# Kernel optimization log

Measured on AMD Instinct MI355X. Metric: run time of the kernel, lower is better.

## Reference

```python
import jax, jax.numpy as jnp
import numpy as np
from jax.scipy.special import xlogy

B, N, F_IN, D, L = 32, 512, 20, 128, 5
NEG = -1e7


def setup_inputs() -> dict:
    key = jax.random.key(0)
    ks = jax.random.split(key, 24)
    s = lambda n: 1.0 / np.sqrt(n)
    inp = {}
    inp["fatoms"] = jax.random.normal(ks[0], (B, N, F_IN), jnp.float32)
    # normalized dense multi-relation adjacency (row sums ~1 for stability)
    inp["adj"] = jax.random.uniform(ks[1], (B, N, N, 3), jnp.float32) * (2.0 / N)
    inp["all_mask"] = jnp.ones((B, N, 1), jnp.float32)
    inp["current_mask"] = jnp.ones((B, N, 1), jnp.float32)
    inp["prob_mask"] = jnp.ones((B, N, 1), jnp.float32)
    inp["focus"] = jax.random.randint(ks[2], (B, 1), 0, N)
    inp["action_batch"] = jax.random.randint(ks[3], (B, 3), 0, 2)
    # embeddings (bias-free Linear(20, D))
    inp["W_emb"] = jax.random.normal(ks[4], (F_IN, D)) * s(F_IN)
    inp["W_cemb"] = jax.random.normal(ks[5], (F_IN, D)) * s(F_IN)
    # per-iteration, per-relation GCN weights [L,3,D,D] and biases [L,3,D]
    inp["actor_W"] = jax.random.normal(ks[6], (L, 3, D, D)) * s(D)
    inp["actor_b"] = jnp.zeros((L, 3, D), jnp.float32)
    inp["critic_W"] = jax.random.normal(ks[7], (L, 3, D, D)) * s(D)
    inp["critic_b"] = jnp.zeros((L, 3, D), jnp.float32)
    # end_selection_layer: Linear(2D,D)+ReLU+Linear(D,1,no bias)
    inp["We1"] = jax.random.normal(ks[8], (2 * D, D)) * s(2 * D)
    inp["be1"] = jnp.zeros((D,), jnp.float32)
    inp["We2"] = jax.random.normal(ks[9], (D, 1)) * s(D)
    # bond_selection_layer: Linear(2D,D)+ReLU+Linear(D,3,no bias)+Softmax
    inp["Wb1"] = jax.random.normal(ks[10], (2 * D, D)) * s(2 * D)
    inp["bb1"] = jnp.zeros((D,), jnp.float32)
    inp["Wb2"] = jax.random.normal(ks[11], (D, 3)) * s(D)
    # stop_selection_layer: Linear(D,D)+ReLU+Linear(D,2,no bias)+Softmax
    inp["Ws1"] = jax.random.normal(ks[12], (D, D)) * s(D)
    inp["bs1"] = jnp.zeros((D,), jnp.float32)
    inp["Ws2"] = jax.random.normal(ks[13], (D, 2)) * s(D)
    # qlayer: Linear(2D,D)+ReLU+Linear(D,1)
    inp["Wq1"] = jax.random.normal(ks[14], (2 * D, D)) * s(2 * D)
    inp["bq1"] = jnp.zeros((D,), jnp.float32)
    inp["Wq2"] = jax.random.normal(ks[15], (D, 1)) * s(D)
    inp["bq2"] = jnp.zeros((1,), jnp.float32)
    return inp


def _entropy(p):
    return -jnp.sum(xlogy(p, p), axis=-1)


def reference(fatoms, adj, all_mask, current_mask, prob_mask, focus, action_batch,
              W_emb, W_cemb, actor_W, actor_b, critic_W, critic_b,
              We1, be1, We2, Wb1, bb1, Wb2, Ws1, bs1, Ws2, Wq1, bq1, Wq2, bq2):
    def gcn_stack(x, Ws_all, bs_all):
        def step(h, wb):
            W, b = wb  # [3,D,D], [3,D]
            hw = jnp.einsum('bmd,rde->rbme', h, W) + b[:, None, None, :]
            msg = jax.nn.relu(jnp.einsum('bnmr,rbme->rbne', adj, hw))
            return jnp.sum(msg, axis=0) * all_mask, None
        h, _ = jax.lax.scan(step, x, (Ws_all, bs_all))
        return h

    # actor and critic feature updates
    x_a = gcn_stack(jax.nn.relu(fatoms @ W_emb), actor_W, actor_b)   # [B,N,D]
    x_c = gcn_stack(jax.nn.relu(fatoms @ W_cemb), critic_W, critic_b)

    # maxpool_sumpool + qlayer
    max_mask = jnp.where(current_mask == 1.0, 0.0, NEG)
    sum_pool = jnp.sum(x_c * current_mask, axis=1)                   # [B,D]
    max_pool = jnp.max(x_c + max_mask, axis=1)                       # [B,D]
    q_in = jnp.concatenate([sum_pool, max_pool], axis=-1)            # [B,2D]
    qvalue = jax.nn.relu(q_in @ Wq1 + bq1) @ Wq2 + bq2               # [B,1]

    pm = jnp.where(prob_mask == 1.0, 0.0, NEG)                       # [B,N,1]
    b, n, d = x_a.shape
    start = jnp.take_along_axis(x_a, jnp.broadcast_to(focus[:, :, None], (b, 1, d)), axis=1)  # [B,1,D]

    end_input = jnp.concatenate([jnp.broadcast_to(start, (b, n, d)), x_a], axis=-1)           # [B,N,2D]
    logits = jax.nn.relu(end_input @ We1 + be1) @ We2 + pm           # [B,N,1]
    end_probs = jax.nn.softmax(logits, axis=1)[..., 0]               # [B,N]

    end_idx = action_batch[:, 0:1]
    end_atom = jnp.take_along_axis(x_a, jnp.broadcast_to(end_idx[:, :, None], (b, 1, d)), axis=1)
    end_prob_new = jnp.take_along_axis(end_probs, end_idx, axis=1)   # [B,1]

    bond_in = jnp.concatenate([start, end_atom], axis=-1)[:, 0, :]   # [B,2D]
    bond_probs = jax.nn.softmax(jax.nn.relu(bond_in @ Wb1 + bb1) @ Wb2, axis=-1)  # [B,3]
    bond_prob_new = jnp.take_along_axis(bond_probs, action_batch[:, 1:2], axis=1)

    stop_probs = jax.nn.softmax(jax.nn.relu(start[:, 0, :] @ Ws1 + bs1) @ Ws2, axis=-1)  # [B,2]
    stop_prob_new = jnp.take_along_axis(stop_probs, action_batch[:, 2:3], axis=1)

    prob_batch_new = jnp.concatenate([end_prob_new, bond_prob_new, stop_prob_new], axis=-1)  # [B,3]
    entropy = _entropy(end_probs) + _entropy(bond_probs) + _entropy(stop_probs)             # [B]
    return prob_batch_new, entropy, qvalue
```

## Files before the change

kernel.cpp:

```cpp
#include <hip/hip_runtime.h>
#include <cstdint>
#include <cstddef>

typedef unsigned short u16;
typedef __bf16 bfx8 __attribute__((ext_vector_type(8)));
typedef float f32x4 __attribute__((ext_vector_type(4)));

#define NEGV -10000000.0f
constexpr int cB = 32, cN = 512, cD = 128, cF = 20, cL = 5;

__device__ __forceinline__ float bf2f(u16 h){ unsigned u = ((unsigned)h)<<16; return __builtin_bit_cast(float,u); }
__device__ __forceinline__ u16 f2bf(float f){ unsigned u = __builtin_bit_cast(unsigned,f); return (u16)((u + 0x7fffu + ((u>>16)&1u))>>16); }

constexpr int WOF_EMB  = 0;
constexpr int WOF_CEMB = 2560;
constexpr int WOF_AW   = 5120;
constexpr int WOF_CW   = 250880;
constexpr int WOF_WE1  = 496640;
constexpr int WOF_WE2  = 529408;
constexpr int WOF_WB1  = 529536;
constexpr int WOF_WB2  = 562304;
constexpr int WOF_WS1  = 562688;
constexpr int WOF_WS2  = 579072;
constexpr int WOF_WQ1  = 579328;
constexpr int WOF_WQ2  = 612096;
constexpr int WTOTAL   = 612224;

struct WPtrs { const void* p[12]; };

__global__ __launch_bounds__(256) void canon_w(WPtrs wp, u16* __restrict__ Wc){
  __shared__ int s_flag;
  int t = threadIdx.x;
  if (t == 0) s_flag = 0;
  __syncthreads();
  const u16* probe = (const u16*)wp.p[2];
  int big = 0;
  #pragma unroll
  for (int i=0;i<2;++i){
    float a = fabsf(bf2f(probe[i*256 + t]));
    if (!(a < 1e10f)) big = 1;
  }
  if (__any(big)) s_flag = 1;
  __syncthreads();
  int flag = s_flag;
  int i = blockIdx.x*256 + t;
  if (i >= WTOTAL) return;
  constexpr int offs[13] = {WOF_EMB, WOF_CEMB, WOF_AW, WOF_CW, WOF_WE1, WOF_WE2,
                            WOF_WB1, WOF_WB2, WOF_WS1, WOF_WS2, WOF_WQ1, WOF_WQ2, WTOTAL};
  int a = 0;
  #pragma unroll
  for (int k = 1; k < 12; ++k) if (i >= offs[k]) a = k;
  int off = i - offs[a];
  const void* p = wp.p[a];
  Wc[i] = flag ? f2bf(((const float*)p)[off]) : ((const u16*)p)[off];
}

__global__ __launch_bounds__(256) void prep_adj(const float* __restrict__ adj, u16* __restrict__ adjT){
  int idx = blockIdx.x*256 + threadIdx.x;
  int m8 = idx & 63; int bn = idx >> 6;
  const float* src = adj + ((size_t)bn*512 + (size_t)m8*8)*3;
  float v[24];
  #pragma unroll
  for (int q=0;q<6;++q) ((float4*)v)[q] = ((const float4*)src)[q];
  __align__(16) u16 o[3][8];
  #pragma unroll
  for (int j=0;j<24;++j) o[j%3][j/3] = f2bf(v[j]);
  #pragma unroll
  for (int r=0;r<3;++r){
    size_t off = ((size_t)r*16384 + (size_t)bn)*512 + (size_t)m8*8;
    *reinterpret_cast<int4*>(adjT + off) = *reinterpret_cast<const int4*>(&o[r][0]);
  }
}

__global__ __launch_bounds__(256) void prep_w(const u16* __restrict__ Wc, u16* __restrict__ WT){
  __shared__ u16 sh[128*129];
  int blk = blockIdx.x;
  const u16* in;
  if (blk < 30){
    int s = blk/15; int lr = blk%15;
    in = Wc + (s ? WOF_CW : WOF_AW) + (size_t)lr*16384;
  } else {
    in = Wc + WOF_WE1 + 128*cD;
  }
  u16* out = WT + (size_t)blk*16384;
  int t = threadIdx.x;
  #pragma unroll 4
  for (int i=0;i<64;++i){ int idx=i*256+t; int d=idx>>7, e=idx&127; sh[e*129+d]=in[idx]; }
  __syncthreads();
  #pragma unroll 4
  for (int i=0;i<64;++i){ int idx=i*256+t; int e=idx>>7, d=idx&127; out[idx]=sh[e*129+d]; }
}

__global__ __launch_bounds__(128) void emb(const float* __restrict__ fatoms, const u16* __restrict__ Wc, u16* __restrict__ h0){
  int row = blockIdx.x;
  int s = row >> 14; int bn = row & 16383;
  __shared__ float fa[cF];
  int t = threadIdx.x;
  if (t < cF) fa[t] = fatoms[(size_t)bn*cF + t];
  __syncthreads();
  const u16* W = Wc + (s ? WOF_CEMB : WOF_EMB);
  float acc = 0.f;
  #pragma unroll
  for (int f=0; f<cF; ++f) acc += fa[f]*bf2f(W[f*cD + t]);
  h0[((size_t)s*cB*cN + bn)*cD + t] = f2bf(fmaxf(acc,0.f));
}

__device__ __forceinline__ void stage16k(const u16* gbase, int ldaB, int ktB, char* sm, int w, int l){
  #pragma unroll
  for (int i=0;i<4;++i){
    int c = (w<<2) + i;
    int row = (c<<3) + (l>>3);
    const char* src = (const char*)gbase + (size_t)row*ldaB + ktB + (((l&7)^(row&7))<<4);
    __builtin_amdgcn_global_load_lds((const __attribute__((address_space(1))) void*)src,
                                     (__attribute__((address_space(3))) void*)(sm + (c<<10)), 16, 0, 0);
  }
}
__device__ __forceinline__ void stage8k(const u16* gbase, int ldaB, int ktB, char* sm, int w, int l){
  #pragma unroll
  for (int i=0;i<2;++i){
    int c = (w<<1) + i;
    int row = (c<<3) + (l>>3);
    const char* src = (const char*)gbase + (size_t)row*ldaB + ktB + (((l&7)^(row&7))<<4);
    __builtin_amdgcn_global_load_lds((const __attribute__((address_space(1))) void*)src,
                                     (__attribute__((address_space(3))) void*)(sm + (c<<10)), 16, 0, 0);
  }
}
__device__ __forceinline__ bfx8 readfrag(const char* sm, int row, int kk, int l){
  int col = ((kk<<6) + ((l>>4)<<4)) ^ ((row&7)<<4);
  return *(const bfx8*)(sm + row*128 + col);
}
template<int MF,int NF>
__device__ __forceinline__ void mfma_tile(const char* A, const char* Bm, int ra, int rb, int l, f32x4 (&acc)[MF][NF]){
  #pragma unroll
  for (int kk=0; kk<2; ++kk){
    bfx8 af[MF], bv[NF];
    #pragma unroll
    for (int f=0; f<MF; ++f) af[f] = readfrag(A,  ra+(f<<4)+(l&15), kk, l);
    #pragma unroll
    for (int f=0; f<NF; ++f) bv[f] = readfrag(Bm, rb+(f<<4)+(l&15), kk, l);
    #pragma unroll
    for (int mf=0; mf<MF; ++mf)
      #pragma unroll
      for (int nf=0; nf<NF; ++nf)
        acc[mf][nf] = __builtin_amdgcn_mfma_f32_16x16x32_bf16(af[mf], bv[nf], acc[mf][nf], 0,0,0);
  }
}

__global__ __launch_bounds__(256,2) void k1_hw(const u16* __restrict__ WT, const u16* __restrict__ h,
                                               const float* __restrict__ actor_b, const float* __restrict__ critic_b,
                                               u16* __restrict__ hwT, int layer){
  __shared__ __align__(16) char smA[16384];
  __shared__ __align__(16) char smB[16384];
  int blk = blockIdx.x;
  int nt = blk & 3; int srb = blk >> 2;
  int s = srb/96; int rb = srb%96; int r = rb>>5; int b = rb&31;
  int t = threadIdx.x, w = t>>6, l = t&63, wr = w>>1, wc = w&1;
  const u16* Abase = WT + (size_t)(s*15 + layer*3 + r)*16384;
  const u16* Bbase = h + ((size_t)s*cB*cN + (size_t)b*cN + (size_t)nt*128)*cD;
  f32x4 acc[4][4];
  #pragma unroll
  for (int i=0;i<4;++i){ acc[i][0]=f32x4{0,0,0,0}; acc[i][1]=f32x4{0,0,0,0}; acc[i][2]=f32x4{0,0,0,0}; acc[i][3]=f32x4{0,0,0,0}; }
  for (int kt=0; kt<2; ++kt){
    __syncthreads();
    stage16k(Abase, 256, kt*128, smA, w, l);
    stage16k(Bbase, 256, kt*128, smB, w, l);
    __syncthreads();
    mfma_tile<4,4>(smA, smB, wr<<6, wc<<6, l, acc);
  }
  const float* bias = (s ? critic_b : actor_b) + (layer*3 + r)*cD;
  u16* outB = hwT + (size_t)((s*3+r)*cB + b)*cD*cN;
  #pragma unroll
  for (int mf=0; mf<4; ++mf)
    #pragma unroll
    for (int nf=0; nf<4; ++nf)
      #pragma unroll
      for (int j=0; j<4; ++j){
        int e = (wr<<6) + (mf<<4) + ((l>>4)<<2) + j;
        int m = nt*128 + (wc<<6) + (nf<<4) + (l&15);
        outB[(size_t)e*cN + m] = f2bf(acc[mf][nf][j] + bias[e]);
      }
}

__global__ __launch_bounds__(256,2) void k2f(const u16* __restrict__ adjT, const u16* __restrict__ hwT_in,
                                             u16* __restrict__ hwT_out, const float* __restrict__ all_mask,
                                             const u16* __restrict__ WT,
                                             const float* __restrict__ actor_b, const float* __restrict__ critic_b,
                                             u16* __restrict__ hfin, int layer){
  __shared__ __align__(16) char smA[8192];
  __shared__ __align__(16) char smB[16384];
  __shared__ __align__(16) char smW[16384];
  __shared__ __align__(16) char hT[2][8192];
  int blk = blockIdx.x;
  int xcd = blk & 7; int slot = blk >> 3;
  int b = (slot>>4)*8 + xcd;
  int rest = slot & 15; int s = rest>>3; int mt = rest&7;
  int t = threadIdx.x, w = t>>6, l = t&63, wr = w>>1, wc = w&1;
  f32x4 sum[2][4];
  #pragma unroll
  for (int i=0;i<2;++i)
    #pragma unroll
    for (int j=0;j<4;++j) sum[i][j]=f32x4{0,0,0,0};
  for (int r=0; r<3; ++r){
    f32x4 acc[2][4];
    #pragma unroll
    for (int i=0;i<2;++i)
      #pragma unroll
      for (int j=0;j<4;++j) acc[i][j]=f32x4{0,0,0,0};
    const u16* Abase = adjT + ((size_t)(r*cB + b)*cN + (size_t)mt*64)*cN;
    const u16* Bbase = hwT_in + (size_t)((s*3+r)*cB + b)*cD*cN;
    for (int kt=0; kt<8; ++kt){
      __syncthreads();
      stage8k (Abase, 1024, kt*128, smA, w, l);
      stage16k(Bbase, 1024, kt*128, smB, w, l);
      __syncthreads();
      mfma_tile<2,4>(smA, smB, wr<<5, wc<<6, l, acc);
    }
    #pragma unroll
    for (int mf=0; mf<2; ++mf)
      #pragma unroll
      for (int nf=0; nf<4; ++nf)
        #pragma unroll
        for (int j=0; j<4; ++j)
          sum[mf][nf][j] += fmaxf(acc[mf][nf][j], 0.f);
  }
  #pragma unroll
  for (int mf=0; mf<2; ++mf)
    #pragma unroll
    for (int nf=0; nf<4; ++nf)
      #pragma unroll
      for (int j=0; j<4; ++j){
        int nl = (wr<<5) + (mf<<4) + ((l>>4)<<2) + j;
        int e  = (wc<<6) + (nf<<4) + (l&15);
        int n  = mt*64 + nl;
        u16 hv = f2bf(sum[mf][nf][j] * all_mask[b*cN + n]);
        char* dst = hT[e>>6] + nl*128 + (((e&63)*2) ^ ((nl&7)<<4));
        *(u16*)dst = hv;
        if (layer == cL-1) hfin[((size_t)(s*cB + b)*cN + n)*cD + e] = hv;
      }
  if (layer < cL-1){
    for (int r=0; r<3; ++r){
      __syncthreads();
      const u16* Wbase = WT + (size_t)(s*15 + (layer+1)*3 + r)*16384;
      stage16k(Wbase, 256, 0,   smB, w, l);
      stage16k(Wbase, 256, 128, smW, w, l);
      __syncthreads();
      f32x4 acc2[4][2];
      #pragma unroll
      for (int i=0;i<4;++i){ acc2[i][0]=f32x4{0,0,0,0}; acc2[i][1]=f32x4{0,0,0,0}; }
      mfma_tile<4,2>(smB, hT[0], wr<<6, wc<<5, l, acc2);
      mfma_tile<4,2>(smW, hT[1], wr<<6, wc<<5, l, acc2);
      const float* bias = (s ? critic_b : actor_b) + ((layer+1)*3 + r)*cD;
      u16* outB = hwT_out + (size_t)((s*3+r)*cB + b)*cD*cN;
      #pragma unroll
      for (int mf=0; mf<4; ++mf)
        #pragma unroll
        for (int nf=0; nf<2; ++nf)
          #pragma unroll
          for (int j=0; j<4; ++j){
            int e = (wr<<6) + (mf<<4) + ((l>>4)<<2) + j;
            int m = mt*64 + (wc<<5) + (nf<<4) + (l&15);
            outB[(size_t)e*cN + m] = f2bf(acc2[mf][nf][j] + bias[e]);
          }
    }
  }
}

__global__ __launch_bounds__(256) void pool_part(const u16* __restrict__ xc, const float* __restrict__ cmask,
                                                 float* __restrict__ part){
  int blk = blockIdx.x;
  int b = blk >> 4, c = blk & 15;
  int t = threadIdx.x; int d = t & 127, nh = t >> 7;
  const u16* x = xc + ((size_t)b*cN + c*32 + nh*16)*cD;
  const float* cm = cmask + (size_t)b*cN + c*32 + nh*16;
  float sm = 0.f, mx = -3e38f;
  #pragma unroll
  for (int i=0;i<16;++i){
    float v = bf2f(x[(size_t)i*cD + d]);
    float m = cm[i];
    sm += v*m;
    mx = fmaxf(mx, v + (m==1.0f ? 0.f : NEGV));
  }
  __shared__ float s_sm[2][128], s_mx[2][128];
  s_sm[nh][d] = sm; s_mx[nh][d] = mx;
  __syncthreads();
  if (nh == 0){
    float* dst = part + ((size_t)b*16 + c)*256;
    dst[d]       = sm + s_sm[1][d];
    dst[128 + d] = fmaxf(mx, s_mx[1][d]);
  }
}

__global__ __launch_bounds__(128) void start_vec(const u16* __restrict__ xa, const int* __restrict__ focus,
                                                 const int* __restrict__ action, const u16* __restrict__ Wc,
                                                 const float* __restrict__ be1,
                                                 float* __restrict__ startv, float* __restrict__ endv, float* __restrict__ sc){
  int b = blockIdx.x, t = threadIdx.x;
  __shared__ float s_sh[128];
  const u16* We1 = Wc + WOF_WE1;
  int f = focus[b];
  int e0 = action[b*3 + 0];
  float sv = bf2f(xa[((size_t)b*cN + f)*cD + t]);
  startv[b*cD + t] = sv;
  endv[b*cD + t] = bf2f(xa[((size_t)b*cN + e0)*cD + t]);
  s_sh[t] = sv;
  __syncthreads();
  float acc = be1[t];
  #pragma unroll 4
  for (int k=0;k<128;++k) acc += s_sh[k]*bf2f(We1[k*cD + t]);
  sc[b*cD + t] = acc;
}

__global__ __launch_bounds__(256,2) void end_logits2(const u16* __restrict__ xa, const u16* __restrict__ WT,
                                                     const float* __restrict__ sc, const u16* __restrict__ Wc,
                                                     const float* __restrict__ prob_mask, float* __restrict__ logits){
  __shared__ __align__(16) char smA[16384];
  __shared__ __align__(16) char smB[16384];
  __shared__ float sh_sc[128], sh_w2[128], rowsum[2][128];
  int blk = blockIdx.x;
  int nt = blk & 3, b = blk >> 2;
  int t = threadIdx.x, w = t>>6, l = t&63, wr = w>>1, wc = w&1;
  if (t < 128){ sh_sc[t] = sc[b*cD + t]; sh_w2[t] = bf2f(Wc[WOF_WE2 + t]); }
  const u16* Abase = xa + ((size_t)b*cN + (size_t)nt*128)*cD;
  const u16* Bbase = WT + (size_t)30*16384;
  f32x4 acc[4][4];
  #pragma unroll
  for (int i=0;i<4;++i){ acc[i][0]=f32x4{0,0,0,0}; acc[i][1]=f32x4{0,0,0,0}; acc[i][2]=f32x4{0,0,0,0}; acc[i][3]=f32x4{0,0,0,0}; }
  for (int kt=0; kt<2; ++kt){
    __syncthreads();
    stage16k(Abase, 256, kt*128, smA, w, l);
    stage16k(Bbase, 256, kt*128, smB, w, l);
    __syncthreads();
    mfma_tile<4,4>(smA, smB, wr<<6, wc<<6, l, acc);
  }
  float p[4][4];
  #pragma unroll
  for (int mf=0;mf<4;++mf)
    #pragma unroll
    for (int j=0;j<4;++j) p[mf][j] = 0.f;
  #pragma unroll
  for (int mf=0; mf<4; ++mf)
    #pragma unroll
    for (int nf=0; nf<4; ++nf){
      int e = (wc<<6) + (nf<<4) + (l&15);
      float scv = sh_sc[e], w2 = sh_w2[e];
      #pragma unroll
      for (int j=0; j<4; ++j)
        p[mf][j] += fmaxf(acc[mf][nf][j] + scv, 0.f) * w2;
    }
  #pragma unroll
  for (int mf=0; mf<4; ++mf)
    #pragma unroll
    for (int j=0; j<4; ++j){
      float v = p[mf][j];
      #pragma unroll
      for (int o=1;o<16;o<<=1) v += __shfl_xor(v, o, 64);
      if ((l&15)==0) rowsum[wc][(wr<<6) + (mf<<4) + ((l>>4)<<2) + j] = v;
    }
  __syncthreads();
  if (t < 128){
    int n = nt*128 + t;
    float pm = (prob_mask[b*cN + n]==1.0f) ? 0.f : NEGV;
    logits[b*cN + n] = rowsum[0][t] + rowsum[1][t] + pm;
  }
}

__global__ __launch_bounds__(128) void heads_final(const float* __restrict__ part, const u16* __restrict__ Wc,
                                                   const float* __restrict__ bq1, const float* __restrict__ bq2,
                                                   const float* __restrict__ logits, const int* __restrict__ action,
                                                   const float* __restrict__ startv, const float* __restrict__ endv,
                                                   const float* __restrict__ bb1, const float* __restrict__ bs1,
                                                   float* __restrict__ out){
  int b = blockIdx.x, t = threadIdx.x;
  __shared__ float qin[256];
  __shared__ float sv[128], ev[128];
  __shared__ float redq[2], red5[5][2];
  __shared__ float HendSh;
  sv[t] = startv[b*cD + t];
  ev[t] = endv[b*cD + t];
  float sm = 0.f, mx = -3e38f;
  #pragma unroll
  for (int c=0;c<16;++c){
    const float* src = part + ((size_t)b*16 + c)*256;
    sm += src[t];
    mx = fmaxf(mx, src[128 + t]);
  }
  qin[t] = sm; qin[128+t] = mx;
  __syncthreads();
  float acc = bq1[t];
  #pragma unroll 4
  for (int k=0; k<256; ++k) acc += qin[k]*bf2f(Wc[WOF_WQ1 + k*cD + t]);
  float hc = fmaxf(acc,0.f)*bf2f(Wc[WOF_WQ2 + t]);
  #pragma unroll
  for (int o=32;o>0;o>>=1) hc += __shfl_down(hc, o, 64);
  if ((t&63)==0) redq[t>>6] = hc;
  if (t < 64){
    float v[8];
    #pragma unroll
    for (int i=0;i<8;++i) v[i] = logits[b*cN + i*64 + t];
    float m = v[0];
    #pragma unroll
    for (int i=1;i<8;++i) m = fmaxf(m, v[i]);
    #pragma unroll
    for (int o=32;o>0;o>>=1) m = fmaxf(m, __shfl_xor(m, o, 64));
    float e[8]; float s = 0.f;
    #pragma unroll
    for (int i=0;i<8;++i){ e[i] = expf(v[i]-m); s += e[i]; }
    #pragma unroll
    for (int o=32;o>0;o>>=1) s += __shfl_xor(s, o, 64);
    float lns = logf(s);
    float pl = 0.f;
    #pragma unroll
    for (int i=0;i<8;++i){ float p = e[i]/s; pl += p*((v[i]-m) - lns); }
    #pragma unroll
    for (int o=32;o>0;o>>=1) pl += __shfl_xor(pl, o, 64);
    int idx = action[b*3 + 0];
    if (t == (idx & 63)){
      float pe = 0.f;
      #pragma unroll
      for (int i=0;i<8;++i) if ((idx>>6)==i) pe = e[i];
      out[b*3 + 0] = pe / s;
    }
    if (t == 0) HendSh = -pl;
  }
  float ab = bb1[t], as_ = bs1[t];
  #pragma unroll 4
  for (int k=0;k<128;++k){ float svk = sv[k]; ab += svk*bf2f(Wc[WOF_WB1 + k*cD + t]); as_ += svk*bf2f(Wc[WOF_WS1 + k*cD + t]); }
  #pragma unroll 4
  for (int k=0;k<128;++k) ab += ev[k]*bf2f(Wc[WOF_WB1 + (128+k)*cD + t]);
  float hb = fmaxf(ab,0.f), hs = fmaxf(as_,0.f);
  float r0 = hb*bf2f(Wc[WOF_WB2 + t*3+0]);
  float r1 = hb*bf2f(Wc[WOF_WB2 + t*3+1]);
  float r2 = hb*bf2f(Wc[WOF_WB2 + t*3+2]);
  float r3 = hs*bf2f(Wc[WOF_WS2 + t*2+0]);
  float r4 = hs*bf2f(Wc[WOF_WS2 + t*2+1]);
  #pragma unroll
  for (int o=32;o>0;o>>=1){
    r0 += __shfl_xor(r0,o,64); r1 += __shfl_xor(r1,o,64); r2 += __shfl_xor(r2,o,64);
    r3 += __shfl_xor(r3,o,64); r4 += __shfl_xor(r4,o,64);
  }
  if ((t&63)==0){ int wid=t>>6; red5[0][wid]=r0; red5[1][wid]=r1; red5[2][wid]=r2; red5[3][wid]=r3; red5[4][wid]=r4; }
  __syncthreads();
  if (t==0){
    out[128 + b] = redq[0] + redq[1] + bq2[0];
    auto xlx = [](float p){ return p > 0.f ? p*logf(p) : 0.f; };
    float bl0=red5[0][0]+red5[0][1], bl1=red5[1][0]+red5[1][1], bl2=red5[2][0]+red5[2][1];
    float sl0=red5[3][0]+red5[3][1], sl1=red5[4][0]+red5[4][1];
    float m = fmaxf(fmaxf(bl0,bl1),bl2);
    float e0=expf(bl0-m), e1=expf(bl1-m), e2=expf(bl2-m); float S=e0+e1+e2;
    float p0=e0/S, p1=e1/S, p2=e2/S;
    float Hb = -(xlx(p0) + xlx(p1) + xlx(p2));
    int a1 = action[b*3+1];
    out[b*3+1] = (a1==0)?p0:((a1==1)?p1:p2);
    float ms = fmaxf(sl0,sl1);
    float f0=expf(sl0-ms), f1=expf(sl1-ms); float T=f0+f1;
    float q0=f0/T, q1=f1/T;
    float Hs = -(xlx(q0) + xlx(q1));
    int a2 = action[b*3+2];
    out[b*3+2] = (a2==0)?q0:q1;
    out[96+b] = HendSh + Hb + Hs;
  }
}

extern "C" void kernel_launch(void* const* d_in, const int* in_sizes, int n_in,
                              void* d_out, int out_size, void* d_ws, size_t ws_size,
                              hipStream_t stream){
  const float* fatoms      = (const float*)d_in[0];
  const float* adj         = (const float*)d_in[1];
  const float* all_mask    = (const float*)d_in[2];
  const float* current_mask= (const float*)d_in[3];
  const float* prob_mask   = (const float*)d_in[4];
  const int*   focus       = (const int*)d_in[5];
  const int*   action      = (const int*)d_in[6];
  const float* actor_b     = (const float*)d_in[10];
  const float* critic_b    = (const float*)d_in[12];
  const float* be1         = (const float*)d_in[14];
  const float* bb1         = (const float*)d_in[17];
  const float* bs1         = (const float*)d_in[20];
  const float* bq1         = (const float*)d_in[23];
  const float* bq2         = (const float*)d_in[25];

  char* ws = (char*)d_ws;
  size_t o = 0;
  u16* adjT = (u16*)(ws + o);  o += (size_t)3*cB*cN*cN*2;
  u16* WT   = (u16*)(ws + o);  o += (size_t)31*16384*2;
  u16* hbuf = (u16*)(ws + o);  o += (size_t)2*2*cB*cN*cD*2;
  u16* hwT0 = (u16*)(ws + o);  o += (size_t)2*3*cB*cD*cN*2;
  u16* hwT1 = (u16*)(ws + o);  o += (size_t)2*3*cB*cD*cN*2;
  u16* Wcan = (u16*)(ws + o);  o += (size_t)WTOTAL*2;
  float* part   = (float*)(ws + o); o += (size_t)cB*16*256*4;
  float* logits = (float*)(ws + o); o += (size_t)cB*cN*4;
  float* sc     = (float*)(ws + o); o += (size_t)cB*cD*4;
  float* startv = (float*)(ws + o); o += (size_t)cB*cD*4;
  float* endv   = (float*)(ws + o); o += (size_t)cB*cD*4;
  float* out = (float*)d_out;

  WPtrs wp;
  wp.p[0]=d_in[7];  wp.p[1]=d_in[8];  wp.p[2]=d_in[9];  wp.p[3]=d_in[11];
  wp.p[4]=d_in[13]; wp.p[5]=d_in[15]; wp.p[6]=d_in[16]; wp.p[7]=d_in[18];
  wp.p[8]=d_in[19]; wp.p[9]=d_in[21]; wp.p[10]=d_in[22]; wp.p[11]=d_in[24];

  canon_w<<<dim3((WTOTAL+255)/256), dim3(256), 0, stream>>>(wp, Wcan);
  prep_adj<<<dim3(4096), dim3(256), 0, stream>>>(adj, adjT);
  prep_w<<<dim3(31), dim3(256), 0, stream>>>(Wcan, WT);
  emb<<<dim3(2*cB*cN), dim3(128), 0, stream>>>(fatoms, Wcan, hbuf);

  const size_t hstride = (size_t)2*cB*cN*cD;
  u16* hfin = hbuf + hstride;
  k1_hw<<<dim3(768), dim3(256), 0, stream>>>(WT, hbuf, actor_b, critic_b, hwT0, 0);
  for (int l=0; l<cL; ++l){
    u16* win  = (l&1) ? hwT1 : hwT0;
    u16* wout = (l&1) ? hwT0 : hwT1;
    k2f<<<dim3(512), dim3(256), 0, stream>>>(adjT, win, wout, all_mask, WT, actor_b, critic_b, hfin, l);
  }
  const u16* xa = hfin;
  const u16* xc = hfin + (size_t)cB*cN*cD;

  start_vec<<<dim3(cB), dim3(128), 0, stream>>>(xa, focus, action, Wcan, be1, startv, endv, sc);
  end_logits2<<<dim3(cB*4), dim3(256), 0, stream>>>(xa, WT, sc, Wcan, prob_mask, logits);
  pool_part<<<dim3(cB*16), dim3(256), 0, stream>>>(xc, current_mask, part);
  heads_final<<<dim3(cB), dim3(128), 0, stream>>>(part, Wcan, bq1, bq2, logits, action, startv, endv, bb1, bs1, out);
}
```

Before: 260.0 us.

## Double-buffer adjacency and hw tiles in k2f with async staged loads

Flattens the three relation loops and eight k-tiles in k2f into one 24-step loop. The shared tiles become two buffers, so global loads for the next tile are issued before the MFMA work on the current one, using explicit vmcnt waits and raw barriers in place of __syncthreads. The weight-staging phase reuses the now double-sized smB buffer instead of a separate smW, which keeps LDS usage roughly the same. This relies on stage8k/stage16k issuing exactly the expected number of vector memory ops for vmcnt(6) to be correct, so a mismatch would cause data races.

```diff
diff --git a/kernel.cpp b/kernel.cpp
--- a/kernel.cpp
+++ b/kernel.cpp
@@ -186,42 +186,52 @@
                                              const u16* __restrict__ WT,
                                              const float* __restrict__ actor_b, const float* __restrict__ critic_b,
                                              u16* __restrict__ hfin, int layer){
-  __shared__ __align__(16) char smA[8192];
-  __shared__ __align__(16) char smB[16384];
-  __shared__ __align__(16) char smW[16384];
+  __shared__ __align__(16) char smA[2][8192];
+  __shared__ __align__(16) char smB[2][16384];
   __shared__ __align__(16) char hT[2][8192];
   int blk = blockIdx.x;
   int xcd = blk & 7; int slot = blk >> 3;
   int b = (slot>>4)*8 + xcd;
   int rest = slot & 15; int s = rest>>3; int mt = rest&7;
   int t = threadIdx.x, w = t>>6, l = t&63, wr = w>>1, wc = w&1;
-  f32x4 sum[2][4];
+  const u16* adjB = adjT + ((size_t)b*cN + (size_t)mt*64)*cN;
+  const u16* hwB  = hwT_in + (size_t)(s*3*cB + b)*cD*cN;
+  const size_t adjRs = (size_t)cB*cN*cN;
+  const size_t hwRs  = (size_t)cB*cD*cN;
+  f32x4 sum[2][4], acc[2][4];
   #pragma unroll
   for (int i=0;i<2;++i)
     #pragma unroll
-    for (int j=0;j<4;++j) sum[i][j]=f32x4{0,0,0,0};
-  for (int r=0; r<3; ++r){
-    f32x4 acc[2][4];
-    #pragma unroll
-    for (int i=0;i<2;++i)
-      #pragma unroll
-      for (int j=0;j<4;++j) acc[i][j]=f32x4{0,0,0,0};
-    const u16* Abase = adjT + ((size_t)(r*cB + b)*cN + (size_t)mt*64)*cN;
-    const u16* Bbase = hwT_in + (size_t)((s*3+r)*cB + b)*cD*cN;
-    for (int kt=0; kt<8; ++kt){
-      __syncthreads();
-      stage8k (Abase, 1024, kt*128, smA, w, l);
-      stage16k(Bbase, 1024, kt*128, smB, w, l);
-      __syncthreads();
-      mfma_tile<2,4>(smA, smB, wr<<5, wc<<6, l, acc);
+    for (int j=0;j<4;++j){ sum[i][j]=f32x4{0,0,0,0}; acc[i][j]=f32x4{0,0,0,0}; }
+  stage8k (adjB, 1024, 0, smA[0], w, l);
+  stage16k(hwB,  1024, 0, smB[0], w, l);
+  #pragma unroll
+  for (int p=0; p<24; ++p){
+    const int cur = p & 1;
+    if (p < 23){
+      const int pn = p + 1, rn = pn >> 3, ktb = (pn & 7) * 128;
+      stage8k (adjB + (size_t)rn*adjRs, 1024, ktb, smA[cur^1], w, l);
+      stage16k(hwB  + (size_t)rn*hwRs,  1024, ktb, smB[cur^1], w, l);
+      asm volatile("s_waitcnt vmcnt(6)" ::: "memory");
+    } else {
+      asm volatile("s_waitcnt vmcnt(0)" ::: "memory");
     }
-    #pragma unroll
-    for (int mf=0; mf<2; ++mf)
-      #pragma unroll
-      for (int nf=0; nf<4; ++nf)
+    __builtin_amdgcn_s_barrier();
+    __builtin_amdgcn_sched_barrier(0);
+    mfma_tile<2,4>(smA[cur], smB[cur], wr<<5, wc<<6, l, acc);
+    if ((p & 7) == 7){
+      #pragma unroll
+      for (int mf=0; mf<2; ++mf)
         #pragma unroll
-        for (int j=0; j<4; ++j)
-          sum[mf][nf][j] += fmaxf(acc[mf][nf][j], 0.f);
+        for (int nf=0; nf<4; ++nf)
+          #pragma unroll
+          for (int j=0; j<4; ++j){
+            sum[mf][nf][j] += fmaxf(acc[mf][nf][j], 0.f);
+            acc[mf][nf][j] = 0.f;
+          }
+    }
+    __builtin_amdgcn_sched_barrier(0);
+    __builtin_amdgcn_s_barrier();
   }
   #pragma unroll
   for (int mf=0; mf<2; ++mf)
@@ -238,17 +248,22 @@
         if (layer == cL-1) hfin[((size_t)(s*cB + b)*cN + n)*cD + e] = hv;
       }
   if (layer < cL-1){
+    asm volatile("s_waitcnt lgkmcnt(0)" ::: "memory");
+    #pragma unroll
     for (int r=0; r<3; ++r){
-      __syncthreads();
       const u16* Wbase = WT + (size_t)(s*15 + (layer+1)*3 + r)*16384;
-      stage16k(Wbase, 256, 0,   smB, w, l);
-      stage16k(Wbase, 256, 128, smW, w, l);
-      __syncthreads();
+      stage16k(Wbase, 256, 0,   smB[0], w, l);
+      stage16k(Wbase, 256, 128, smB[1], w, l);
+      asm volatile("s_waitcnt vmcnt(0)" ::: "memory");
+      __builtin_amdgcn_s_barrier();
+      __builtin_amdgcn_sched_barrier(0);
       f32x4 acc2[4][2];
       #pragma unroll
       for (int i=0;i<4;++i){ acc2[i][0]=f32x4{0,0,0,0}; acc2[i][1]=f32x4{0,0,0,0}; }
-      mfma_tile<4,2>(smB, hT[0], wr<<6, wc<<5, l, acc2);
-      mfma_tile<4,2>(smW, hT[1], wr<<6, wc<<5, l, acc2);
+      mfma_tile<4,2>(smB[0], hT[0], wr<<6, wc<<5, l, acc2);
+      mfma_tile<4,2>(smB[1], hT[1], wr<<6, wc<<5, l, acc2);
+      __builtin_amdgcn_sched_barrier(0);
+      __builtin_amdgcn_s_barrier();
       const float* bias = (s ? critic_b : actor_b) + ((layer+1)*3 + r)*cD;
       u16* outB = hwT_out + (size_t)((s*3+r)*cB + b)*cD*cN;
       #pragma unroll
```

Result: no change. 260.8 us (+0.3%).

## Fuse adjacency bf16 conversion into first GCN layer and inline start-vector head

Applied to the files above, without the earlier changes.

Drops the standalone prep_adj pass. The first propagation layer now reads the fp32 adjacency directly, converts it to bf16 in shared memory, and processes all three relations in one k-loop. The s==0 blocks also write the bf16 transposed copy for later layers. The start_vec kernel is removed as well: its matvec moves into end_logits2, and heads_final reads the start and end rows directly. This saves two launches and an extra global round trip for the adjacency. The cost is a larger unified 72KB LDS pool and duplicated fp32 adjacency reads by the actor and critic blocks.

```diff
diff --git a/kernel.cpp b/kernel.cpp
--- a/kernel.cpp
+++ b/kernel.cpp
@@ -55,23 +55,6 @@
   Wc[i] = flag ? f2bf(((const float*)p)[off]) : ((const u16*)p)[off];
 }
 
-__global__ __launch_bounds__(256) void prep_adj(const float* __restrict__ adj, u16* __restrict__ adjT){
-  int idx = blockIdx.x*256 + threadIdx.x;
-  int m8 = idx & 63; int bn = idx >> 6;
-  const float* src = adj + ((size_t)bn*512 + (size_t)m8*8)*3;
-  float v[24];
-  #pragma unroll
-  for (int q=0;q<6;++q) ((float4*)v)[q] = ((const float4*)src)[q];
-  __align__(16) u16 o[3][8];
-  #pragma unroll
-  for (int j=0;j<24;++j) o[j%3][j/3] = f2bf(v[j]);
-  #pragma unroll
-  for (int r=0;r<3;++r){
-    size_t off = ((size_t)r*16384 + (size_t)bn)*512 + (size_t)m8*8;
-    *reinterpret_cast<int4*>(adjT + off) = *reinterpret_cast<const int4*>(&o[r][0]);
-  }
-}
-
 __global__ __launch_bounds__(256) void prep_w(const u16* __restrict__ Wc, u16* __restrict__ WT){
   __shared__ u16 sh[128*129];
   int blk = blockIdx.x;
@@ -181,74 +164,130 @@
       }
 }
 
-__global__ __launch_bounds__(256,2) void k2f(const u16* __restrict__ adjT, const u16* __restrict__ hwT_in,
-                                             u16* __restrict__ hwT_out, const float* __restrict__ all_mask,
-                                             const u16* __restrict__ WT,
+template<int L0>
+__global__ __launch_bounds__(256,2) void k2f(const float* __restrict__ adj, u16* __restrict__ adjT,
+                                             const u16* __restrict__ hwT_in, u16* __restrict__ hwT_out,
+                                             const float* __restrict__ all_mask, const u16* __restrict__ WT,
                                              const float* __restrict__ actor_b, const float* __restrict__ critic_b,
                                              u16* __restrict__ hfin, int layer){
-  __shared__ __align__(16) char smA[8192];
-  __shared__ __align__(16) char smB[16384];
-  __shared__ __align__(16) char smW[16384];
-  __shared__ __align__(16) char hT[2][8192];
+  __shared__ __align__(16) char pool[73728];
   int blk = blockIdx.x;
   int xcd = blk & 7; int slot = blk >> 3;
   int b = (slot>>4)*8 + xcd;
   int rest = slot & 15; int s = rest>>3; int mt = rest&7;
   int t = threadIdx.x, w = t>>6, l = t&63, wr = w>>1, wc = w&1;
+  const u16* hwB = hwT_in + (size_t)(s*3*cB + b)*cD*cN;
+  const size_t hwRs = (size_t)cB*cD*cN;
   f32x4 sum[2][4];
   #pragma unroll
   for (int i=0;i<2;++i)
     #pragma unroll
     for (int j=0;j<4;++j) sum[i][j]=f32x4{0,0,0,0};
-  for (int r=0; r<3; ++r){
-    f32x4 acc[2][4];
-    #pragma unroll
-    for (int i=0;i<2;++i)
-      #pragma unroll
-      for (int j=0;j<4;++j) acc[i][j]=f32x4{0,0,0,0};
-    const u16* Abase = adjT + ((size_t)(r*cB + b)*cN + (size_t)mt*64)*cN;
-    const u16* Bbase = hwT_in + (size_t)((s*3+r)*cB + b)*cD*cN;
+
+  if constexpr (L0){
+    f32x4 a3[3][2][4];
+    #pragma unroll
+    for (int r=0;r<3;++r)
+      #pragma unroll
+      for (int i=0;i<2;++i)
+        #pragma unroll
+        for (int j=0;j<4;++j) a3[r][i][j]=f32x4{0,0,0,0};
+    const int nl  = t>>2;
+    const int m8  = (t&3)*2;
+    const float* asrc = adj + ((size_t)(b*cN + mt*64 + nl)*cN + m8*8)*3;
     for (int kt=0; kt<8; ++kt){
+      stage16k(hwB,        1024, kt*128, pool+24576, w, l);
+      stage16k(hwB+hwRs,   1024, kt*128, pool+40960, w, l);
+      stage16k(hwB+2*hwRs, 1024, kt*128, pool+57344, w, l);
+      float4 v[12];
+      const float* sp = asrc + (size_t)kt*64*3;
+      #pragma unroll
+      for (int q=0;q<12;++q) v[q] = ((const float4*)sp)[q];
       __syncthreads();
-      stage8k (Abase, 1024, kt*128, smA, w, l);
-      stage16k(Bbase, 1024, kt*128, smB, w, l);
+      const float* vf = (const float*)v;
+      #pragma unroll
+      for (int i=0;i<2;++i){
+        int m8i = m8 + i;
+        #pragma unroll
+        for (int r=0;r<3;++r){
+          __align__(16) u16 o[8];
+          #pragma unroll
+          for (int k=0;k<8;++k) o[k] = f2bf(vf[i*24 + k*3 + r]);
+          *(int4*)(pool + r*8192 + nl*128 + ((m8i*16) ^ ((nl&7)<<4))) = *(const int4*)o;
+          if (s == 0)
+            *(int4*)(adjT + ((size_t)(r*cB + b)*cN + mt*64 + nl)*cN + kt*64 + m8i*8) = *(const int4*)o;
+        }
+      }
       __syncthreads();
-      mfma_tile<2,4>(smA, smB, wr<<5, wc<<6, l, acc);
+      #pragma unroll
+      for (int r=0;r<3;++r)
+        mfma_tile<2,4>(pool + r*8192, pool + 24576 + r*16384, wr<<5, wc<<6, l, a3[r]);
     }
     #pragma unroll
-    for (int mf=0; mf<2; ++mf)
-      #pragma unroll
-      for (int nf=0; nf<4; ++nf)
+    for (int r=0;r<3;++r)
+      #pragma unroll
+      for (int mf=0;mf<2;++mf)
         #pragma unroll
-        for (int j=0; j<4; ++j)
-          sum[mf][nf][j] += fmaxf(acc[mf][nf][j], 0.f);
-  }
+        for (int nf=0;nf<4;++nf)
+          #pragma unroll
+          for (int j=0;j<4;++j)
+            sum[mf][nf][j] += fmaxf(a3[r][mf][nf][j], 0.f);
+  } else {
+    const u16* adjB = adjT + ((size_t)b*cN + (size_t)mt*64)*cN;
+    const size_t adjRs = (size_t)cB*cN*cN;
+    for (int r=0;r<3;++r){
+      f32x4 acc[2][4];
+      #pragma unroll
+      for (int i=0;i<2;++i)
+        #pragma unroll
+        for (int j=0;j<4;++j) acc[i][j]=f32x4{0,0,0,0};
+      for (int kt=0;kt<8;++kt){
+        __syncthreads();
+        stage8k (adjB + (size_t)r*adjRs, 1024, kt*128, pool, w, l);
+        stage16k(hwB  + (size_t)r*hwRs,  1024, kt*128, pool+8192, w, l);
+        __syncthreads();
+        mfma_tile<2,4>(pool, pool+8192, wr<<5, wc<<6, l, acc);
+      }
+      #pragma unroll
+      for (int mf=0;mf<2;++mf)
+        #pragma unroll
+        for (int nf=0;nf<4;++nf)
+          #pragma unroll
+          for (int j=0;j<4;++j)
+            sum[mf][nf][j] += fmaxf(acc[mf][nf][j], 0.f);
+    }
+  }
+  __syncthreads();
+  char* hT0 = pool + (L0 ? 0 : 24576);
+  char* hT1 = hT0 + 8192;
   #pragma unroll
   for (int mf=0; mf<2; ++mf)
     #pragma unroll
     for (int nf=0; nf<4; ++nf)
       #pragma unroll
       for (int j=0; j<4; ++j){
-        int nl = (wr<<5) + (mf<<4) + ((l>>4)<<2) + j;
-        int e  = (wc<<6) + (nf<<4) + (l&15);
-        int n  = mt*64 + nl;
+        int nloc = (wr<<5) + (mf<<4) + ((l>>4)<<2) + j;
+        int e    = (wc<<6) + (nf<<4) + (l&15);
+        int n    = mt*64 + nloc;
         u16 hv = f2bf(sum[mf][nf][j] * all_mask[b*cN + n]);
-        char* dst = hT[e>>6] + nl*128 + (((e&63)*2) ^ ((nl&7)<<4));
-        *(u16*)dst = hv;
+        char* base = (e & 64) ? hT1 : hT0;
+        *(u16*)(base + nloc*128 + (((e&63)*2) ^ ((nloc&7)<<4))) = hv;
         if (layer == cL-1) hfin[((size_t)(s*cB + b)*cN + n)*cD + e] = hv;
       }
   if (layer < cL-1){
+    char* W0 = pool + (L0 ? 24576 : 40960);
+    char* W1 = W0 + 16384;
     for (int r=0; r<3; ++r){
       __syncthreads();
       const u16* Wbase = WT + (size_t)(s*15 + (layer+1)*3 + r)*16384;
-      stage16k(Wbase, 256, 0,   smB, w, l);
-      stage16k(Wbase, 256, 128, smW, w, l);
+      stage16k(Wbase, 256, 0,   W0, w, l);
+      stage16k(Wbase, 256, 128, W1, w, l);
       __syncthreads();
       f32x4 acc2[4][2];
       #pragma unroll
       for (int i=0;i<4;++i){ acc2[i][0]=f32x4{0,0,0,0}; acc2[i][1]=f32x4{0,0,0,0}; }
-      mfma_tile<4,2>(smB, hT[0], wr<<6, wc<<5, l, acc2);
-      mfma_tile<4,2>(smW, hT[1], wr<<6, wc<<5, l, acc2);
+      mfma_tile<4,2>(W0, hT0, wr<<6, wc<<5, l, acc2);
+      mfma_tile<4,2>(W1, hT1, wr<<6, wc<<5, l, acc2);
       const float* bias = (s ? critic_b : actor_b) + ((layer+1)*3 + r)*cD;
       u16* outB = hwT_out + (size_t)((s*3+r)*cB + b)*cD*cN;
       #pragma unroll
@@ -290,36 +329,27 @@
   }
 }
 
-__global__ __launch_bounds__(128) void start_vec(const u16* __restrict__ xa, const int* __restrict__ focus,
-                                                 const int* __restrict__ action, const u16* __restrict__ Wc,
-                                                 const float* __restrict__ be1,
-                                                 float* __restrict__ startv, float* __restrict__ endv, float* __restrict__ sc){
-  int b = blockIdx.x, t = threadIdx.x;
-  __shared__ float s_sh[128];
-  const u16* We1 = Wc + WOF_WE1;
-  int f = focus[b];
-  int e0 = action[b*3 + 0];
-  float sv = bf2f(xa[((size_t)b*cN + f)*cD + t]);
-  startv[b*cD + t] = sv;
-  endv[b*cD + t] = bf2f(xa[((size_t)b*cN + e0)*cD + t]);
-  s_sh[t] = sv;
-  __syncthreads();
-  float acc = be1[t];
-  #pragma unroll 4
-  for (int k=0;k<128;++k) acc += s_sh[k]*bf2f(We1[k*cD + t]);
-  sc[b*cD + t] = acc;
-}
-
 __global__ __launch_bounds__(256,2) void end_logits2(const u16* __restrict__ xa, const u16* __restrict__ WT,
-                                                     const float* __restrict__ sc, const u16* __restrict__ Wc,
+                                                     const u16* __restrict__ Wc, const int* __restrict__ focus,
+                                                     const float* __restrict__ be1,
                                                      const float* __restrict__ prob_mask, float* __restrict__ logits){
   __shared__ __align__(16) char smA[16384];
   __shared__ __align__(16) char smB[16384];
-  __shared__ float sh_sc[128], sh_w2[128], rowsum[2][128];
+  __shared__ float s_start[128], sh_sc[128], sh_w2[128], rowsum[2][128];
   int blk = blockIdx.x;
   int nt = blk & 3, b = blk >> 2;
   int t = threadIdx.x, w = t>>6, l = t&63, wr = w>>1, wc = w&1;
-  if (t < 128){ sh_sc[t] = sc[b*cD + t]; sh_w2[t] = bf2f(Wc[WOF_WE2 + t]); }
+  if (t < 128){
+    s_start[t] = bf2f(xa[((size_t)b*cN + focus[b])*cD + t]);
+    sh_w2[t]   = bf2f(Wc[WOF_WE2 + t]);
+  }
+  __syncthreads();
+  if (t < 128){
+    float a = be1[t];
+    #pragma unroll 4
+    for (int k=0;k<128;++k) a += s_start[k]*bf2f(Wc[WOF_WE1 + k*cD + t]);
+    sh_sc[t] = a;
+  }
   const u16* Abase = xa + ((size_t)b*cN + (size_t)nt*128)*cD;
   const u16* Bbase = WT + (size_t)30*16384;
   f32x4 acc[4][4];
@@ -367,7 +397,7 @@
 __global__ __launch_bounds__(128) void heads_final(const float* __restrict__ part, const u16* __restrict__ Wc,
                                                    const float* __restrict__ bq1, const float* __restrict__ bq2,
                                                    const float* __restrict__ logits, const int* __restrict__ action,
-                                                   const float* __restrict__ startv, const float* __restrict__ endv,
+                                                   const u16* __restrict__ xa, const int* __restrict__ focus,
                                                    const float* __restrict__ bb1, const float* __restrict__ bs1,
                                                    float* __restrict__ out){
   int b = blockIdx.x, t = threadIdx.x;
@@ -375,8 +405,8 @@
   __shared__ float sv[128], ev[128];
   __shared__ float redq[2], red5[5][2];
   __shared__ float HendSh;
-  sv[t] = startv[b*cD + t];
-  ev[t] = endv[b*cD + t];
+  sv[t] = bf2f(xa[((size_t)b*cN + focus[b])*cD + t]);
+  ev[t] = bf2f(xa[((size_t)b*cN + action[b*3])*cD + t]);
   float sm = 0.f, mx = -3e38f;
   #pragma unroll
   for (int c=0;c<16;++c){
@@ -422,6 +452,7 @@
     }
     if (t == 0) HendSh = -pl;
   }
+  __syncthreads();
   float ab = bb1[t], as_ = bs1[t];
   #pragma unroll 4
   for (int k=0;k<128;++k){ float svk = sv[k]; ab += svk*bf2f(Wc[WOF_WB1 + k*cD + t]); as_ += svk*bf2f(Wc[WOF_WS1 + k*cD + t]); }
@@ -489,9 +520,6 @@
   u16* Wcan = (u16*)(ws + o);  o += (size_t)WTOTAL*2;
   float* part   = (float*)(ws + o); o += (size_t)cB*16*256*4;
   float* logits = (float*)(ws + o); o += (size_t)cB*cN*4;
-  float* sc     = (float*)(ws + o); o += (size_t)cB*cD*4;
-  float* startv = (float*)(ws + o); o += (size_t)cB*cD*4;
-  float* endv   = (float*)(ws + o); o += (size_t)cB*cD*4;
   float* out = (float*)d_out;
 
   WPtrs wp;
@@ -500,23 +528,22 @@
   wp.p[8]=d_in[19]; wp.p[9]=d_in[21]; wp.p[10]=d_in[22]; wp.p[11]=d_in[24];
 
   canon_w<<<dim3((WTOTAL+255)/256), dim3(256), 0, stream>>>(wp, Wcan);
-  prep_adj<<<dim3(4096), dim3(256), 0, stream>>>(adj, adjT);
   prep_w<<<dim3(31), dim3(256), 0, stream>>>(Wcan, WT);
   emb<<<dim3(2*cB*cN), dim3(128), 0, stream>>>(fatoms, Wcan, hbuf);
 
   const size_t hstride = (size_t)2*cB*cN*cD;
   u16* hfin = hbuf + hstride;
   k1_hw<<<dim3(768), dim3(256), 0, stream>>>(WT, hbuf, actor_b, critic_b, hwT0, 0);
-  for (int l=0; l<cL; ++l){
+  k2f<1><<<dim3(512), dim3(256), 0, stream>>>(adj, adjT, hwT0, hwT1, all_mask, WT, actor_b, critic_b, hfin, 0);
+  for (int l=1; l<cL; ++l){
     u16* win  = (l&1) ? hwT1 : hwT0;
     u16* wout = (l&1) ? hwT0 : hwT1;
-    k2f<<<dim3(512), dim3(256), 0, stream>>>(adjT, win, wout, all_mask, WT, actor_b, critic_b, hfin, l);
+    k2f<0><<<dim3(512), dim3(256), 0, stream>>>(adj, adjT, win, wout, all_mask, WT, actor_b, critic_b, hfin, l);
   }
   const u16* xa = hfin;
   const u16* xc = hfin + (size_t)cB*cN*cD;
 
-  start_vec<<<dim3(cB), dim3(128), 0, stream>>>(xa, focus, action, Wcan, be1, startv, endv, sc);
-  end_logits2<<<dim3(cB*4), dim3(256), 0, stream>>>(xa, WT, sc, Wcan, prob_mask, logits);
+  end_logits2<<<dim3(cB*4), dim3(256), 0, stream>>>(xa, WT, Wcan, focus, be1, prob_mask, logits);
   pool_part<<<dim3(cB*16), dim3(256), 0, stream>>>(xc, current_mask, part);
-  heads_final<<<dim3(cB), dim3(128), 0, stream>>>(part, Wcan, bq1, bq2, logits, action, startv, endv, bb1, bs1, out);
-}
+  heads_final<<<dim3(cB), dim3(128), 0, stream>>>(part, Wcan, bq1, bq2, logits, action, xa, focus, bb1, bs1, out);
+}
```

New measurement: 258.8 us. No clear change (-0.4%).
